# Kernel optimization log

Measured on AMD Instinct MI355X. Metric: run time of the kernel, lower is better.

Reference implementation:

```python
import jax, jax.numpy as jnp
import numpy as np

EMBED_DIM = 1024
NUM_HEADS = 16
HEAD_DIM = EMBED_DIM // NUM_HEADS
B, T = 4, 2048


def quantum_layer(x):
    # Exact closed form of the RY + CNOT-chain + PauliZ circuit:
    # expval(Z_i) = prod_{j<=i} cos(x_j)  (cumulative product along feature dim)
    return jnp.cumprod(jnp.cos(x), axis=-1)


def separate_heads(x):
    b, s, _ = x.shape
    return x.reshape(b, s, NUM_HEADS, HEAD_DIM).transpose(0, 2, 1, 3)  # (B,H,T,D)


def combine_heads(x):
    b, h, s, d = x.shape
    return x.transpose(0, 2, 1, 3).reshape(b, s, h * d)


def setup_inputs() -> dict:
    key = jax.random.key(0)
    ks = jax.random.split(key, 9)
    scale = 1.0 / np.sqrt(EMBED_DIM)
    return {
        "x": jax.random.normal(ks[0], (B, T, EMBED_DIM), dtype=jnp.float32),
        "Wq": jax.random.normal(ks[1], (EMBED_DIM, EMBED_DIM), dtype=jnp.float32) * scale,
        "bq": jax.random.normal(ks[2], (EMBED_DIM,), dtype=jnp.float32) * 0.01,
        "Wk": jax.random.normal(ks[3], (EMBED_DIM, EMBED_DIM), dtype=jnp.float32) * scale,
        "bk": jax.random.normal(ks[4], (EMBED_DIM,), dtype=jnp.float32) * 0.01,
        "Wv": jax.random.normal(ks[5], (EMBED_DIM, EMBED_DIM), dtype=jnp.float32) * scale,
        "bv": jax.random.normal(ks[6], (EMBED_DIM,), dtype=jnp.float32) * 0.01,
        "Wo": jax.random.normal(ks[7], (EMBED_DIM, EMBED_DIM), dtype=jnp.float32) * scale,
        "bo": jax.random.normal(ks[8], (EMBED_DIM,), dtype=jnp.float32) * 0.01,
    }


def reference(x, Wq, bq, Wk, bk, Wv, bv, Wo, bo):
    k = x @ Wk + bk
    q = x @ Wq + bq
    v = x @ Wv + bv
    # quantum circuit applied to q and k projections
    q = quantum_layer(q)
    k = quantum_layer(k)
    # NOTE: source swaps roles: kqv = (heads(k), heads(q), heads(v)); q, h, v = kqv
    qh = separate_heads(k)   # acts as query
    kh = separate_heads(q)   # acts as key
    vh = separate_heads(v)
    scores = jnp.einsum("bhqd,bhkd->bhqk", qh, kh) / jnp.sqrt(jnp.float32(HEAD_DIM))
    attn = jax.nn.softmax(scores, axis=-1)  # dropout is identity in eval
    out = jnp.einsum("bhqk,bhkd->bhqd", attn, vh)
    return combine_heads(out) @ Wo + bo
```

## Files before the change

kernel.cpp:

```cpp
#include <hip/hip_runtime.h>
#include <hip/hip_bf16.h>
#include <stdint.h>

#define B_ 4
#define T_ 2048
#define E_ 1024
#define H_ 16
#define D_ 64
#define M_ (B_ * T_)

typedef unsigned short u16;
typedef unsigned int u32;
typedef short s16x8 __attribute__((ext_vector_type(8)));
typedef unsigned short u16x8 __attribute__((ext_vector_type(8)));
typedef float f32x4 __attribute__((ext_vector_type(4)));
typedef unsigned int u32x2 __attribute__((ext_vector_type(2)));

__device__ __forceinline__ u16 f2bf(float f) {
    __hip_bfloat16 h = __float2bfloat16(f);
    return __builtin_bit_cast(u16, h);
}
__device__ __forceinline__ float bf2f(u16 u) {
    unsigned int v = ((unsigned int)u) << 16;
    return __builtin_bit_cast(float, v);
}
__device__ __forceinline__ u32 pk2(float a, float b) {
    return (u32)f2bf(a) | ((u32)f2bf(b) << 16);
}

typedef __attribute__((address_space(1))) const void as1_void;
typedef __attribute__((address_space(3))) void as3_void;
__device__ __forceinline__ void gload16(const void* g, void* l) {
    __builtin_amdgcn_global_load_lds(
        reinterpret_cast<as1_void*>(reinterpret_cast<uintptr_t>(g)),
        reinterpret_cast<as3_void*>(reinterpret_cast<uintptr_t>(l)),
        16, 0, 0);
}

__device__ __forceinline__ int block_probe_is_bf16(const void* x, int tid) {
    const u16* p = (const u16*)x;
    u16 u = p[tid];
    int e = (u >> 7) & 0xFF;
    int ok = ((u & 0x7FFF) == 0 || (e >= 103 && e <= 133)) ? 1 : 0;
    return (__syncthreads_count(ok) >= 240) ? 1 : 0;
}

__global__ __launch_bounds__(256) void transpose_w_single_kernel(
    const void* __restrict__ w0, const void* __restrict__ w1,
    u16* __restrict__ o0, u16* __restrict__ o1,
    const void* __restrict__ xprobe)
{
    __shared__ u16 th[64][66];
    const int x = threadIdx.x, y = threadIdx.y;
    const int isbf = block_probe_is_bf16(xprobe, y * 64 + x);
    const void* in = blockIdx.z ? w1 : w0;
    u16* o = blockIdx.z ? o1 : o0;
    const int r0 = blockIdx.y * 64;
    const int c0 = blockIdx.x * 64;
    #pragma unroll
    for (int j = 0; j < 16; j++) {
        const size_t idx = (size_t)(r0 + y * 16 + j) * E_ + c0 + x;
        float v = isbf ? bf2f(((const u16*)in)[idx]) : ((const float*)in)[idx];
        th[y * 16 + j][x] = f2bf(v);
    }
    __syncthreads();
    #pragma unroll
    for (int j = 0; j < 16; j++)
        o[(size_t)(c0 + y * 16 + j) * E_ + r0 + x] = th[x][y * 16 + j];
}

__global__ __launch_bounds__(256) void convert_bias_kernel(
    const void* __restrict__ bq, const void* __restrict__ bk,
    const void* __restrict__ bv, const void* __restrict__ bo,
    float* __restrict__ outb, const void* __restrict__ xprobe)
{
    const int isbf = block_probe_is_bf16(xprobe, threadIdx.x);
    const int i = blockIdx.x * 256 + threadIdx.x;
    const int w = blockIdx.y;
    const void* p = (w == 0) ? bq : (w == 1) ? bk : (w == 2) ? bv : bo;
    float v = isbf ? bf2f(((const u16*)p)[i]) : ((const float*)p)[i];
    outb[w * 1024 + i] = v;
}

__global__ __launch_bounds__(256) void gemm_f32out_kernel(
    const void* __restrict__ A, int a_mode, int m_base,
    const u16* __restrict__ Bt, const float* __restrict__ bias,
    float* __restrict__ Cout, int ldc)
{
    __shared__ u16 a_lds[128 * 64];
    __shared__ u16 b_lds[128 * 64];
    const int tid = threadIdx.x;
    const int isbf = block_probe_is_bf16(A, tid);
    const int a_bf = (a_mode < 0) ? isbf : a_mode;
    const int wave = tid >> 6, lane = tid & 63;
    const int lane15 = lane & 15, quad = lane >> 4;
    const int wm = (wave & 1) * 64, wn = (wave >> 1) * 64;
    const int nwg = (int)(gridDim.x * gridDim.y);
    const int lin = (int)(blockIdx.y * gridDim.x + blockIdx.x);
    const int swz = (lin & 7) * (nwg >> 3) + (lin >> 3);
    const int m0 = (swz / (int)gridDim.x) * 128;
    const int n0 = (swz % (int)gridDim.x) * 128;

    f32x4 acc[4][4];
    #pragma unroll
    for (int i = 0; i < 4; i++)
        #pragma unroll
        for (int j = 0; j < 4; j++) acc[i][j] = (f32x4)0.0f;

    const int g_r = wave * 32 + (lane >> 3);
    const int g_c = (lane & 7) * 8;
    const u16* ga = (const u16*)A + (size_t)(m_base + m0 + g_r) * E_ + g_c;
    const u16* gb = Bt + (size_t)(n0 + g_r) * E_ + g_c;
    const int srow = tid >> 1;
    const int soff = (tid & 1) * 32;
    const float* abase_f = (const float*)A + (size_t)(m_base + m0 + srow) * E_ + soff;

    for (int kk = 0; kk < E_; kk += 64) {
        __syncthreads();
        if (a_bf) {
            #pragma unroll
            for (int j = 0; j < 4; j++)
                gload16(ga + (size_t)j * 8 * E_ + kk, &a_lds[(wave * 4 + j) * 512]);
        } else {
            #pragma unroll
            for (int j = 0; j < 4; j++) {
                f32x4 t0 = *(const f32x4*)(abase_f + kk + j * 8);
                f32x4 t1 = *(const f32x4*)(abase_f + kk + j * 8 + 4);
                u16x8 o;
                #pragma unroll
                for (int e = 0; e < 4; e++) { o[e] = f2bf(t0[e]); o[4 + e] = f2bf(t1[e]); }
                *(u16x8*)&a_lds[srow * 64 + soff + j * 8] = o;
            }
        }
        #pragma unroll
        for (int j = 0; j < 4; j++)
            gload16(gb + (size_t)j * 8 * E_ + kk, &b_lds[(wave * 4 + j) * 512]);
        __syncthreads();

        #pragma unroll
        for (int ks = 0; ks < 2; ks++) {
            s16x8 af[4], bfr[4];
            #pragma unroll
            for (int i = 0; i < 4; i++)
                af[i] = *(const s16x8*)&a_lds[(wm + i * 16 + lane15) * 64 + ks * 32 + quad * 8];
            #pragma unroll
            for (int j = 0; j < 4; j++)
                bfr[j] = *(const s16x8*)&b_lds[(wn + j * 16 + lane15) * 64 + ks * 32 + quad * 8];
            #pragma unroll
            for (int i = 0; i < 4; i++)
                #pragma unroll
                for (int j = 0; j < 4; j++)
                    acc[i][j] = __builtin_amdgcn_mfma_f32_16x16x32_bf16(af[i], bfr[j], acc[i][j], 0, 0, 0);
        }
    }

    #pragma unroll
    for (int j = 0; j < 4; j++) {
        const int col = n0 + wn + j * 16 + lane15;
        const float bb = bias[col];
        #pragma unroll
        for (int i = 0; i < 4; i++) {
            const int row = m0 + wm + i * 16 + quad * 4;
            #pragma unroll
            for (int r = 0; r < 4; r++)
                Cout[(size_t)(row + r) * ldc + col] = acc[i][j][r] + bb;
        }
    }
}

__global__ __launch_bounds__(256) void gemm_v_fused_kernel(
    const void* __restrict__ X, const u16* __restrict__ Bt,
    const float* __restrict__ bias, u16* __restrict__ Vt)
{
    __shared__ u16 smem[2 * 128 * 72];
    u16* a_lds = smem;
    u16* b_lds = smem + 128 * 72;
    const int tid = threadIdx.x;
    const int isbf = block_probe_is_bf16(X, tid);
    const int wave = tid >> 6, lane = tid & 63;
    const int lane15 = lane & 15, quad = lane >> 4;
    const int wm = (wave & 1) * 64, wn = (wave >> 1) * 64;
    const int nwg = (int)(gridDim.x * gridDim.y);
    const int lin = (int)(blockIdx.y * gridDim.x + blockIdx.x);
    const int swz = (lin & 7) * (nwg >> 3) + (lin >> 3);
    const int m0 = (swz / (int)gridDim.x) * 128;
    const int n0 = (swz % (int)gridDim.x) * 128;
    const int srow = tid >> 1;
    const int soff = (tid & 1) * 32;

    f32x4 acc[4][4];
    #pragma unroll
    for (int i = 0; i < 4; i++)
        #pragma unroll
        for (int j = 0; j < 4; j++) acc[i][j] = (f32x4)0.0f;

    const u16* abase_bf = (const u16*)X + (size_t)(m0 + srow) * E_ + soff;
    const float* abase_f = (const float*)X + (size_t)(m0 + srow) * E_ + soff;
    const u16* bbase = Bt + (size_t)(n0 + srow) * E_ + soff;

    u16x8 av[4], bv[4];
    if (isbf) {
        #pragma unroll
        for (int j = 0; j < 4; j++) av[j] = *(const u16x8*)(abase_bf + j * 8);
    } else {
        #pragma unroll
        for (int j = 0; j < 4; j++) {
            f32x4 t0 = *(const f32x4*)(abase_f + j * 8);
            f32x4 t1 = *(const f32x4*)(abase_f + j * 8 + 4);
            u16x8 o;
            #pragma unroll
            for (int e = 0; e < 4; e++) { o[e] = f2bf(t0[e]); o[4 + e] = f2bf(t1[e]); }
            av[j] = o;
        }
    }
    #pragma unroll
    for (int j = 0; j < 4; j++) bv[j] = *(const u16x8*)(bbase + j * 8);

    for (int kk = 0; kk < E_; kk += 64) {
        __syncthreads();
        #pragma unroll
        for (int j = 0; j < 4; j++) {
            *(u16x8*)&a_lds[srow * 72 + soff + j * 8] = av[j];
            *(u16x8*)&b_lds[srow * 72 + soff + j * 8] = bv[j];
        }
        __syncthreads();
        if (kk + 64 < E_) {
            const int k2 = kk + 64;
            if (isbf) {
                #pragma unroll
                for (int j = 0; j < 4; j++) av[j] = *(const u16x8*)(abase_bf + k2 + j * 8);
            } else {
                #pragma unroll
                for (int j = 0; j < 4; j++) {
                    f32x4 t0 = *(const f32x4*)(abase_f + k2 + j * 8);
                    f32x4 t1 = *(const f32x4*)(abase_f + k2 + j * 8 + 4);
                    u16x8 o;
                    #pragma unroll
                    for (int e = 0; e < 4; e++) { o[e] = f2bf(t0[e]); o[4 + e] = f2bf(t1[e]); }
                    av[j] = o;
                }
            }
            #pragma unroll
            for (int j = 0; j < 4; j++) bv[j] = *(const u16x8*)(bbase + k2 + j * 8);
        }
        #pragma unroll
        for (int ks = 0; ks < 2; ks++) {
            s16x8 af[4], bfr[4];
            #pragma unroll
            for (int i = 0; i < 4; i++)
                af[i] = *(const s16x8*)&a_lds[(wm + i * 16 + lane15) * 72 + ks * 32 + quad * 8];
            #pragma unroll
            for (int j = 0; j < 4; j++)
                bfr[j] = *(const s16x8*)&b_lds[(wn + j * 16 + lane15) * 72 + ks * 32 + quad * 8];
            #pragma unroll
            for (int i = 0; i < 4; i++)
                #pragma unroll
                for (int j = 0; j < 4; j++)
                    acc[i][j] = __builtin_amdgcn_mfma_f32_16x16x32_bf16(af[i], bfr[j], acc[i][j], 0, 0, 0);
        }
    }

    __syncthreads();
    u16* c_tile = smem;
    #pragma unroll
    for (int j = 0; j < 4; j++) {
        const float bb = bias[n0 + wn + j * 16 + lane15];
        #pragma unroll
        for (int i = 0; i < 4; i++)
            #pragma unroll
            for (int r = 0; r < 4; r++)
                c_tile[(wm + i * 16 + quad * 4 + r) * 132 + wn + j * 16 + lane15] =
                    f2bf(acc[i][j][r] + bb);
    }
    __syncthreads();
    const int b = m0 >> 11, t0 = m0 & 2047;
    const int orow = tid >> 1, half = tid & 1;
    u16* dst = Vt + ((size_t)b * 1024 + n0 + orow) * T_ + t0 + half * 64;
    #pragma unroll
    for (int c = 0; c < 8; c++) {
        u16x8 o;
        #pragma unroll
        for (int e = 0; e < 8; e++)
            o[e] = c_tile[(half * 64 + c * 8 + e) * 132 + orow];
        *(u16x8*)(dst + c * 8) = o;
    }
}

__global__ __launch_bounds__(256) void quantum2_kernel(
    const float* __restrict__ in, u16* __restrict__ key, u16* __restrict__ qry)
{
    const int wave = threadIdx.x >> 6, lane = threadIdx.x & 63;
    const int unit = (int)blockIdx.x * 4 + wave;
    const int row = unit >> 1, seg = unit & 1;
    const float* p = in + (size_t)row * 2048 + seg * 1024 + lane * 16;
    float v[16];
    #pragma unroll
    for (int j = 0; j < 16; j += 4) {
        f32x4 t = *(const f32x4*)(p + j);
        v[j] = t[0]; v[j + 1] = t[1]; v[j + 2] = t[2]; v[j + 3] = t[3];
    }
    float pl[16];
    float run = 1.0f;
    #pragma unroll
    for (int j = 0; j < 16; j++) { run *= cosf(v[j]); pl[j] = run; }
    float incl = run;
    #pragma unroll
    for (int off = 1; off < 64; off <<= 1) {
        float t = __shfl_up(incl, off);
        if (lane >= off) incl *= t;
    }
    float pref = __shfl_up(incl, 1);
    if (lane == 0) pref = 1.0f;
    u16x8 o0, o1;
    #pragma unroll
    for (int j = 0; j < 8; j++) {
        o0[j] = f2bf(pref * pl[j]);
        o1[j] = f2bf(pref * pl[j + 8]);
    }
    u16* outp = (seg ? qry : key) + (size_t)row * E_ + lane * 16;
    *(u16x8*)(outp) = o0;
    *(u16x8*)(outp + 8) = o1;
}

__global__ __launch_bounds__(256) void attn_kernel(
    const u16* __restrict__ Qrm, const u16* __restrict__ Krm,
    const u16* __restrict__ Vt, u16* __restrict__ Orm)
{
    __shared__ u16 k_lds[64 * 72];
    __shared__ u16 v_lds[64 * 72];
    __shared__ u16 p_lds[128 * 72];
    const int tid = threadIdx.x;
    const int wave = tid >> 6, lane = tid & 63;
    const int lane15 = lane & 15, quad = lane >> 4;

    const int lin = (int)(blockIdx.x + gridDim.x * blockIdx.y);
    const int swz = (lin & 7) * 128 + (lin >> 3);
    const int t0 = (swz & 15) * 128;
    const int bh = swz >> 4;
    const int b = bh >> 4, h = bh & 15;

    s16x8 qf[2][2];
    #pragma unroll
    for (int mt = 0; mt < 2; mt++)
        #pragma unroll
        for (int ks = 0; ks < 2; ks++) {
            const u16* src = Qrm
                + (size_t)(b * T_ + t0 + wave * 32 + mt * 16 + lane15) * E_
                + h * 64 + ks * 32 + quad * 8;
            u16x8 t = *(const u16x8*)src;
            u16x8 o;
            #pragma unroll
            for (int e = 0; e < 8; e++) o[e] = f2bf(bf2f(t[e]) * 0.125f);
            qf[mt][ks] = __builtin_bit_cast(s16x8, o);
        }

    f32x4 lsum4[2];
    f32x4 oacc[2][4];
    #pragma unroll
    for (int mt = 0; mt < 2; mt++) {
        lsum4[mt] = (f32x4)0.0f;
        #pragma unroll
        for (int n = 0; n < 4; n++) oacc[mt][n] = (f32x4)0.0f;
    }

    const u16* kbase = Krm + (size_t)(b * T_) * E_ + h * 64;
    const u16* vbase = Vt + (size_t)bh * 64 * T_;
    const int srow = tid >> 2;
    const int soff = (tid & 3) * 16;

    u16x8 kpre0, kpre1, vpre0, vpre1;
    {
        const u16* ksrc = kbase + (size_t)srow * E_ + soff;
        kpre0 = *(const u16x8*)(ksrc);
        kpre1 = *(const u16x8*)(ksrc + 8);
        const u16* vsrc = vbase + (size_t)srow * T_ + soff;
        vpre0 = *(const u16x8*)(vsrc);
        vpre1 = *(const u16x8*)(vsrc + 8);
    }

    for (int tk0 = 0; tk0 < T_; tk0 += 64) {
        __syncthreads();
        *(u16x8*)&k_lds[srow * 72 + soff]     = kpre0;
        *(u16x8*)&k_lds[srow * 72 + soff + 8] = kpre1;
        *(u16x8*)&v_lds[srow * 72 + soff]     = vpre0;
        *(u16x8*)&v_lds[srow * 72 + soff + 8] = vpre1;
        __syncthreads();

        if (tk0 + 64 < T_) {
            const u16* ksrc = kbase + (size_t)(tk0 + 64 + srow) * E_ + soff;
            kpre0 = *(const u16x8*)(ksrc);
            kpre1 = *(const u16x8*)(ksrc + 8);
            const u16* vsrc = vbase + (size_t)srow * T_ + tk0 + 64 + soff;
            vpre0 = *(const u16x8*)(vsrc);
            vpre1 = *(const u16x8*)(vsrc + 8);
        }

        f32x4 sacc[2][4];
        #pragma unroll
        for (int mt = 0; mt < 2; mt++)
            #pragma unroll
            for (int j = 0; j < 4; j++) sacc[mt][j] = (f32x4)0.0f;
        #pragma unroll
        for (int ks = 0; ks < 2; ks++) {
            s16x8 kb[4];
            #pragma unroll
            for (int j = 0; j < 4; j++)
                kb[j] = *(const s16x8*)&k_lds[(j * 16 + lane15) * 72 + ks * 32 + quad * 8];
            #pragma unroll
            for (int mt = 0; mt < 2; mt++)
                #pragma unroll
                for (int j = 0; j < 4; j++)
                    sacc[mt][j] = __builtin_amdgcn_mfma_f32_16x16x32_bf16(
                        kb[j], qf[mt][ks], sacc[mt][j], 0, 0, 0);
        }

        #pragma unroll
        for (int mt = 0; mt < 2; mt++)
            #pragma unroll
            for (int j = 0; j < 4; j++) {
                const f32x4 s = sacc[mt][j];
                const float p0 = __expf(s[0]);
                const float p1 = __expf(s[1]);
                const float p2 = __expf(s[2]);
                const float p3 = __expf(s[3]);
                lsum4[mt][0] += p0; lsum4[mt][1] += p1;
                lsum4[mt][2] += p2; lsum4[mt][3] += p3;
                u32x2 w;
                w[0] = pk2(p0, p1);
                w[1] = pk2(p2, p3);
                *(u32x2*)&p_lds[(wave * 32 + mt * 16 + lane15) * 72 + j * 16 + quad * 4] = w;
            }

        #pragma unroll
        for (int ks = 0; ks < 2; ks++) {
            s16x8 pa[2], vb[4];
            #pragma unroll
            for (int mt = 0; mt < 2; mt++)
                pa[mt] = *(const s16x8*)&p_lds[(wave * 32 + mt * 16 + lane15) * 72 + ks * 32 + quad * 8];
            #pragma unroll
            for (int n = 0; n < 4; n++)
                vb[n] = *(const s16x8*)&v_lds[(n * 16 + lane15) * 72 + ks * 32 + quad * 8];
            #pragma unroll
            for (int mt = 0; mt < 2; mt++)
                #pragma unroll
                for (int n = 0; n < 4; n++)
                    oacc[mt][n] = __builtin_amdgcn_mfma_f32_16x16x32_bf16(
                        pa[mt], vb[n], oacc[mt][n], 0, 0, 0);
        }
    }

    #pragma unroll
    for (int mt = 0; mt < 2; mt++) {
        float l = lsum4[mt][0] + lsum4[mt][1] + lsum4[mt][2] + lsum4[mt][3];
        l += __shfl_xor(l, 16);
        l += __shfl_xor(l, 32);
        #pragma unroll
        for (int r = 0; r < 4; r++) {
            const float lr = __shfl(l, quad * 4 + r);
            const float inv = 1.0f / lr;
            const size_t row = (size_t)(b * T_ + t0 + wave * 32 + mt * 16 + quad * 4 + r);
            #pragma unroll
            for (int n = 0; n < 4; n++)
                Orm[row * E_ + h * 64 + n * 16 + lane15] = f2bf(oacc[mt][n][r] * inv);
        }
    }
}

extern "C" void kernel_launch(void* const* d_in, const int* in_sizes, int n_in,
                              void* d_out, int out_size, void* d_ws, size_t ws_size,
                              hipStream_t stream) {
    (void)in_sizes; (void)n_in; (void)out_size; (void)ws_size;
    const void* x  = d_in[0];
    const void* Wq = d_in[1];
    const void* bq = d_in[2];
    const void* Wk = d_in[3];
    const void* bk = d_in[4];
    const void* Wv = d_in[5];
    const void* bv = d_in[6];
    const void* Wo = d_in[7];
    const void* bo = d_in[8];

    char* ws = (char*)d_ws;
    const size_t MB = 1024 * 1024;
    u16*   wt_o  = (u16*)(ws);
    float* biasf = (float*)(ws + 2 * MB);
    u16*   wt_qk = (u16*)(ws + 3 * MB);
    u16*   wt_v  = (u16*)(ws + 7 * MB);
    u16*   key   = (u16*)(ws + 9 * MB);
    u16*   qry   = (u16*)(ws + 25 * MB);
    float* tmp   = (float*)(ws + 41 * MB);
    u16*   vt    = (u16*)(ws + 41 * MB);
    u16*   orm   = (u16*)(ws + 57 * MB);

    transpose_w_single_kernel<<<dim3(16, 16, 2), dim3(64, 4), 0, stream>>>(
        Wq, Wk, wt_qk, wt_qk + 1024 * 1024, x);
    transpose_w_single_kernel<<<dim3(16, 16, 2), dim3(64, 4), 0, stream>>>(
        Wv, Wo, wt_v, wt_o, x);
    convert_bias_kernel<<<dim3(4, 4), 256, 0, stream>>>(
        bq, bk, bv, bo, biasf, x);

    for (int hh = 0; hh < 2; hh++) {
        gemm_f32out_kernel<<<dim3(16, 32), 256, 0, stream>>>(
            x, -1, hh * 4096, wt_qk, biasf, tmp, 2048);
        quantum2_kernel<<<2048, 256, 0, stream>>>(
            tmp, key + (size_t)hh * 4096 * E_, qry + (size_t)hh * 4096 * E_);
    }

    gemm_v_fused_kernel<<<dim3(8, 64), 256, 0, stream>>>(x, wt_v, biasf + 2 * 1024, vt);

    attn_kernel<<<dim3(16, 64), 256, 0, stream>>>(qry, key, vt, orm);

    gemm_f32out_kernel<<<dim3(8, 64), 256, 0, stream>>>(
        orm, 1, 0, wt_o, biasf + 3 * 1024, (float*)d_out, 1024);
}
```

Before: 419.4 us.

## Fuse QKV projection into one GEMM, double-buffer f32out GEMM, merge weight transposes

Merges the four weight transposes into one launch. Adds a single QKV GEMM over a concatenated transposed weight that writes Q/K in f32 for the quantum kernel and V transposed in bf16, when the workspace is large enough. Double-buffers LDS in gemm_f32out_kernel so the next K-tile loads overlap the MFMAs. The aim is fewer launches, a larger grid for better CU fill, and hidden global-load latency, at the cost of twice the LDS in the output GEMM and a workspace-size-dependent code path.

```diff
diff --git a/kernel.cpp b/kernel.cpp
--- a/kernel.cpp
+++ b/kernel.cpp
@@ -45,16 +45,58 @@
     return (__syncthreads_count(ok) >= 240) ? 1 : 0;
 }
 
-__global__ __launch_bounds__(256) void transpose_w_single_kernel(
+__device__ __forceinline__ void stage_bf(const u16* g, int kk, u16* l, int wave) {
+    #pragma unroll
+    for (int j = 0; j < 4; j++)
+        gload16(g + (size_t)j * 8 * E_ + kk, l + (wave * 4 + j) * 512);
+}
+__device__ __forceinline__ void stage_a_f32(
+    const float* abase_f, int kk, u16* al, int srow, int soff)
+{
+    #pragma unroll
+    for (int j = 0; j < 4; j++) {
+        f32x4 t0 = *(const f32x4*)(abase_f + kk + j * 8);
+        f32x4 t1 = *(const f32x4*)(abase_f + kk + j * 8 + 4);
+        u16x8 o;
+        #pragma unroll
+        for (int e = 0; e < 4; e++) { o[e] = f2bf(t0[e]); o[4 + e] = f2bf(t1[e]); }
+        *(u16x8*)&al[srow * 64 + soff + j * 8] = o;
+    }
+}
+__device__ __forceinline__ void mfma_tile(
+    const u16* al, const u16* bl, f32x4 (&acc)[4][4],
+    int wm, int wn, int lane15, int quad)
+{
+    #pragma unroll
+    for (int ks = 0; ks < 2; ks++) {
+        s16x8 af[4], bfr[4];
+        #pragma unroll
+        for (int i = 0; i < 4; i++)
+            af[i] = *(const s16x8*)&al[(wm + i * 16 + lane15) * 64 + ks * 32 + quad * 8];
+        #pragma unroll
+        for (int j = 0; j < 4; j++)
+            bfr[j] = *(const s16x8*)&bl[(wn + j * 16 + lane15) * 64 + ks * 32 + quad * 8];
+        #pragma unroll
+        for (int i = 0; i < 4; i++)
+            #pragma unroll
+            for (int j = 0; j < 4; j++)
+                acc[i][j] = __builtin_amdgcn_mfma_f32_16x16x32_bf16(af[i], bfr[j], acc[i][j], 0, 0, 0);
+    }
+}
+
+__global__ __launch_bounds__(256) void transpose_w4_kernel(
     const void* __restrict__ w0, const void* __restrict__ w1,
+    const void* __restrict__ w2, const void* __restrict__ w3,
     u16* __restrict__ o0, u16* __restrict__ o1,
+    u16* __restrict__ o2, u16* __restrict__ o3,
     const void* __restrict__ xprobe)
 {
     __shared__ u16 th[64][66];
     const int x = threadIdx.x, y = threadIdx.y;
     const int isbf = block_probe_is_bf16(xprobe, y * 64 + x);
-    const void* in = blockIdx.z ? w1 : w0;
-    u16* o = blockIdx.z ? o1 : o0;
+    const int z = (int)blockIdx.z;
+    const void* in = (z == 0) ? w0 : (z == 1) ? w1 : (z == 2) ? w2 : w3;
+    u16* o = (z == 0) ? o0 : (z == 1) ? o1 : (z == 2) ? o2 : o3;
     const int r0 = blockIdx.y * 64;
     const int c0 = blockIdx.x * 64;
     #pragma unroll
@@ -87,8 +129,8 @@
     const u16* __restrict__ Bt, const float* __restrict__ bias,
     float* __restrict__ Cout, int ldc)
 {
-    __shared__ u16 a_lds[128 * 64];
-    __shared__ u16 b_lds[128 * 64];
+    __shared__ u16 a_lds[2][128 * 64];
+    __shared__ u16 b_lds[2][128 * 64];
     const int tid = threadIdx.x;
     const int isbf = block_probe_is_bf16(A, tid);
     const int a_bf = (a_mode < 0) ? isbf : a_mode;
@@ -115,44 +157,21 @@
     const int soff = (tid & 1) * 32;
     const float* abase_f = (const float*)A + (size_t)(m_base + m0 + srow) * E_ + soff;
 
-    for (int kk = 0; kk < E_; kk += 64) {
-        __syncthreads();
-        if (a_bf) {
-            #pragma unroll
-            for (int j = 0; j < 4; j++)
-                gload16(ga + (size_t)j * 8 * E_ + kk, &a_lds[(wave * 4 + j) * 512]);
-        } else {
-            #pragma unroll
-            for (int j = 0; j < 4; j++) {
-                f32x4 t0 = *(const f32x4*)(abase_f + kk + j * 8);
-                f32x4 t1 = *(const f32x4*)(abase_f + kk + j * 8 + 4);
-                u16x8 o;
-                #pragma unroll
-                for (int e = 0; e < 4; e++) { o[e] = f2bf(t0[e]); o[4 + e] = f2bf(t1[e]); }
-                *(u16x8*)&a_lds[srow * 64 + soff + j * 8] = o;
-            }
-        }
-        #pragma unroll
-        for (int j = 0; j < 4; j++)
-            gload16(gb + (size_t)j * 8 * E_ + kk, &b_lds[(wave * 4 + j) * 512]);
-        __syncthreads();
-
-        #pragma unroll
-        for (int ks = 0; ks < 2; ks++) {
-            s16x8 af[4], bfr[4];
-            #pragma unroll
-            for (int i = 0; i < 4; i++)
-                af[i] = *(const s16x8*)&a_lds[(wm + i * 16 + lane15) * 64 + ks * 32 + quad * 8];
-            #pragma unroll
-            for (int j = 0; j < 4; j++)
-                bfr[j] = *(const s16x8*)&b_lds[(wn + j * 16 + lane15) * 64 + ks * 32 + quad * 8];
-            #pragma unroll
-            for (int i = 0; i < 4; i++)
-                #pragma unroll
-                for (int j = 0; j < 4; j++)
-                    acc[i][j] = __builtin_amdgcn_mfma_f32_16x16x32_bf16(af[i], bfr[j], acc[i][j], 0, 0, 0);
-        }
-    }
+    if (a_bf) stage_bf(ga, 0, a_lds[0], wave);
+    else      stage_a_f32(abase_f, 0, a_lds[0], srow, soff);
+    stage_bf(gb, 0, b_lds[0], wave);
+    __syncthreads();
+
+    for (int t = 0; t < 15; ++t) {
+        const int cur = t & 1, nxt = cur ^ 1;
+        const int kk = (t + 1) * 64;
+        if (a_bf) stage_bf(ga, kk, a_lds[nxt], wave);
+        else      stage_a_f32(abase_f, kk, a_lds[nxt], srow, soff);
+        stage_bf(gb, kk, b_lds[nxt], wave);
+        mfma_tile(a_lds[cur], b_lds[cur], acc, wm, wn, lane15, quad);
+        __syncthreads();
+    }
+    mfma_tile(a_lds[1], b_lds[1], acc, wm, wn, lane15, quad);
 
     #pragma unroll
     for (int j = 0; j < 4; j++) {
@@ -164,6 +183,90 @@
             #pragma unroll
             for (int r = 0; r < 4; r++)
                 Cout[(size_t)(row + r) * ldc + col] = acc[i][j][r] + bb;
+        }
+    }
+}
+
+__global__ __launch_bounds__(256) void gemm_qkv_kernel(
+    const void* __restrict__ A, const u16* __restrict__ Bt,
+    const float* __restrict__ bias, float* __restrict__ Cout,
+    u16* __restrict__ Vt)
+{
+    __shared__ u16 smem[128 * 132];
+    u16* a_l = smem;
+    u16* b_l = smem + 8192;
+    const int tid = threadIdx.x;
+    const int isbf = block_probe_is_bf16(A, tid);
+    const int wave = tid >> 6, lane = tid & 63;
+    const int lane15 = lane & 15, quad = lane >> 4;
+    const int wm = (wave & 1) * 64, wn = (wave >> 1) * 64;
+    const int nwg = (int)(gridDim.x * gridDim.y);
+    const int lin = (int)(blockIdx.y * gridDim.x + blockIdx.x);
+    const int swz = (lin & 7) * (nwg >> 3) + (lin >> 3);
+    const int m0 = (swz / (int)gridDim.x) * 128;
+    const int n0 = (swz % (int)gridDim.x) * 128;
+
+    f32x4 acc[4][4];
+    #pragma unroll
+    for (int i = 0; i < 4; i++)
+        #pragma unroll
+        for (int j = 0; j < 4; j++) acc[i][j] = (f32x4)0.0f;
+
+    const int g_r = wave * 32 + (lane >> 3);
+    const int g_c = (lane & 7) * 8;
+    const u16* ga = (const u16*)A + (size_t)(m0 + g_r) * E_ + g_c;
+    const u16* gb = Bt + (size_t)(n0 + g_r) * E_ + g_c;
+    const int srow = tid >> 1;
+    const int soff = (tid & 1) * 32;
+    const float* abase_f = (const float*)A + (size_t)(m0 + srow) * E_ + soff;
+
+    for (int kk = 0; kk < E_; kk += 64) {
+        __syncthreads();
+        if (isbf) stage_bf(ga, kk, a_l, wave);
+        else      stage_a_f32(abase_f, kk, a_l, srow, soff);
+        stage_bf(gb, kk, b_l, wave);
+        __syncthreads();
+        mfma_tile(a_l, b_l, acc, wm, wn, lane15, quad);
+    }
+
+    if (n0 < 2048) {
+        #pragma unroll
+        for (int j = 0; j < 4; j++) {
+            const int col = n0 + wn + j * 16 + lane15;
+            const float bb = bias[col];
+            #pragma unroll
+            for (int i = 0; i < 4; i++) {
+                const int row = m0 + wm + i * 16 + quad * 4;
+                #pragma unroll
+                for (int r = 0; r < 4; r++)
+                    Cout[(size_t)(row + r) * 2048 + col] = acc[i][j][r] + bb;
+            }
+        }
+    } else {
+        __syncthreads();
+        u16* c_tile = smem;
+        #pragma unroll
+        for (int j = 0; j < 4; j++) {
+            const float bb = bias[n0 + wn + j * 16 + lane15];
+            #pragma unroll
+            for (int i = 0; i < 4; i++)
+                #pragma unroll
+                for (int r = 0; r < 4; r++)
+                    c_tile[(wm + i * 16 + quad * 4 + r) * 132 + wn + j * 16 + lane15] =
+                        f2bf(acc[i][j][r] + bb);
+        }
+        __syncthreads();
+        const int b = m0 >> 11, t0 = m0 & 2047;
+        const int orow = tid >> 1, half = tid & 1;
+        const int n0v = n0 - 2048;
+        u16* dst = Vt + ((size_t)b * 1024 + n0v + orow) * T_ + t0 + half * 64;
+        #pragma unroll
+        for (int c = 0; c < 8; c++) {
+            u16x8 o;
+            #pragma unroll
+            for (int e = 0; e < 8; e++)
+                o[e] = c_tile[(half * 64 + c * 8 + e) * 132 + orow];
+            *(u16x8*)(dst + c * 8) = o;
         }
     }
 }
@@ -469,7 +572,7 @@
 extern "C" void kernel_launch(void* const* d_in, const int* in_sizes, int n_in,
                               void* d_out, int out_size, void* d_ws, size_t ws_size,
                               hipStream_t stream) {
-    (void)in_sizes; (void)n_in; (void)out_size; (void)ws_size;
+    (void)in_sizes; (void)n_in; (void)out_size;
     const void* x  = d_in[0];
     const void* Wq = d_in[1];
     const void* bq = d_in[2];
@@ -482,34 +585,42 @@
 
     char* ws = (char*)d_ws;
     const size_t MB = 1024 * 1024;
-    u16*   wt_o  = (u16*)(ws);
-    float* biasf = (float*)(ws + 2 * MB);
-    u16*   wt_qk = (u16*)(ws + 3 * MB);
-    u16*   wt_v  = (u16*)(ws + 7 * MB);
-    u16*   key   = (u16*)(ws + 9 * MB);
-    u16*   qry   = (u16*)(ws + 25 * MB);
-    float* tmp   = (float*)(ws + 41 * MB);
-    u16*   vt    = (u16*)(ws + 41 * MB);
-    u16*   orm   = (u16*)(ws + 57 * MB);
-
-    transpose_w_single_kernel<<<dim3(16, 16, 2), dim3(64, 4), 0, stream>>>(
-        Wq, Wk, wt_qk, wt_qk + 1024 * 1024, x);
-    transpose_w_single_kernel<<<dim3(16, 16, 2), dim3(64, 4), 0, stream>>>(
-        Wv, Wo, wt_v, wt_o, x);
+    u16*   wt_o   = (u16*)(ws);
+    float* biasf  = (float*)(ws + 2 * MB);
+    u16*   wt_qkv = (u16*)(ws + 3 * MB);
+    u16*   key    = (u16*)(ws + 9 * MB);
+    u16*   qry    = (u16*)(ws + 25 * MB);
+
+    transpose_w4_kernel<<<dim3(16, 16, 4), dim3(64, 4), 0, stream>>>(
+        Wq, Wk, Wv, Wo,
+        wt_qkv, wt_qkv + 1024 * 1024, wt_qkv + 2 * 1024 * 1024, wt_o, x);
     convert_bias_kernel<<<dim3(4, 4), 256, 0, stream>>>(
         bq, bk, bv, bo, biasf, x);
 
-    for (int hh = 0; hh < 2; hh++) {
-        gemm_f32out_kernel<<<dim3(16, 32), 256, 0, stream>>>(
-            x, -1, hh * 4096, wt_qk, biasf, tmp, 2048);
-        quantum2_kernel<<<2048, 256, 0, stream>>>(
-            tmp, key + (size_t)hh * 4096 * E_, qry + (size_t)hh * 4096 * E_);
-    }
-
-    gemm_v_fused_kernel<<<dim3(8, 64), 256, 0, stream>>>(x, wt_v, biasf + 2 * 1024, vt);
-
-    attn_kernel<<<dim3(16, 64), 256, 0, stream>>>(qry, key, vt, orm);
-
-    gemm_f32out_kernel<<<dim3(8, 64), 256, 0, stream>>>(
-        orm, 1, 0, wt_o, biasf + 3 * 1024, (float*)d_out, 1024);
-}
+    if (ws_size >= (size_t)121 * MB) {
+        u16*   vt  = (u16*)(ws + 41 * MB);
+        float* tmp = (float*)(ws + 57 * MB);
+        u16*   orm = (u16*)(ws + 57 * MB);
+        gemm_qkv_kernel<<<dim3(24, 64), 256, 0, stream>>>(
+            x, wt_qkv, biasf, tmp, vt);
+        quantum2_kernel<<<4096, 256, 0, stream>>>(tmp, key, qry);
+        attn_kernel<<<dim3(16, 64), 256, 0, stream>>>(qry, key, vt, orm);
+        gemm_f32out_kernel<<<dim3(8, 64), 256, 0, stream>>>(
+            orm, 1, 0, wt_o, biasf + 3 * 1024, (float*)d_out, 1024);
+    } else {
+        float* tmp = (float*)(ws + 41 * MB);
+        u16*   vt  = (u16*)(ws + 41 * MB);
+        u16*   orm = (u16*)(ws + 57 * MB);
+        for (int hh = 0; hh < 2; hh++) {
+            gemm_f32out_kernel<<<dim3(16, 32), 256, 0, stream>>>(
+                x, -1, hh * 4096, wt_qkv, biasf, tmp, 2048);
+            quantum2_kernel<<<2048, 256, 0, stream>>>(
+                tmp, key + (size_t)hh * 4096 * E_, qry + (size_t)hh * 4096 * E_);
+        }
+        gemm_v_fused_kernel<<<dim3(8, 64), 256, 0, stream>>>(
+            x, wt_qkv + 2 * 1024 * 1024, biasf + 2 * 1024, vt);
+        attn_kernel<<<dim3(16, 64), 256, 0, stream>>>(qry, key, vt, orm);
+        gemm_f32out_kernel<<<dim3(8, 64), 256, 0, stream>>>(
+            orm, 1, 0, wt_o, biasf + 3 * 1024, (float*)d_out, 1024);
+    }
+}
```

Result: faster. 378.6 us (-9.7%).
